# Kernel tuning notes

Measured on AMD Instinct MI355X. Metric: run time of the kernel, lower is better.

The kernel has to match this reference:

```python
import jax, jax.numpy as jnp
import numpy as np

N = 4096
FEAT = 5
H = 128
L = 3
K = 4
HD = H // K  # 32


def setup_inputs() -> dict:
    key = jax.random.key(0)
    ks = jax.random.split(key, 24)
    node_features = jax.random.normal(ks[0], (N, FEAT), dtype=jnp.float32)
    u = jax.random.uniform(ks[1], (N, N), dtype=jnp.float32)
    adj = jnp.where(u < 0.01, u, 0.0)
    adj = adj / (adj.sum(axis=1, keepdims=True) + 1e-8)  # row-normalised
    mask = jax.random.randint(ks[2], (N,), 0, 2).astype(bool)
    s = 0.05
    return {
        'node_features': node_features,
        'adj': adj,
        'mask': mask,
        'Wi': jax.random.normal(ks[3], (FEAT, H), jnp.float32) * s,
        'bi': jnp.zeros((H,), jnp.float32),
        'gat_W': jax.random.normal(ks[4], (L, K, H, HD), jnp.float32) * s,
        'gat_a': jax.random.normal(ks[5], (L, K, 2 * HD), jnp.float32) * s,
        'ln_g': jnp.ones((L, H), jnp.float32),
        'ln_b': jnp.zeros((L, H), jnp.float32),
        'pW1': jax.random.normal(ks[6], (H, H // 2), jnp.float32) * s,
        'pb1': jnp.zeros((H // 2,), jnp.float32),
        'pW2': jax.random.normal(ks[7], (H // 2, 1), jnp.float32) * s,
        'pb2': jnp.zeros((1,), jnp.float32),
        'poolW': jax.random.normal(ks[8], (H, H), jnp.float32) * s,
        'poolb': jnp.zeros((H,), jnp.float32),
        'poolv': jax.random.normal(ks[9], (H,), jnp.float32) * s,
        'vW1': jax.random.normal(ks[10], (H, H // 2), jnp.float32) * s,
        'vb1': jnp.zeros((H // 2,), jnp.float32),
        'vW2': jax.random.normal(ks[11], (H // 2, 1), jnp.float32) * s,
        'vb2': jnp.zeros((1,), jnp.float32),
    }


def _layernorm(x, g, b, eps=1e-5):
    mu = x.mean(-1, keepdims=True)
    var = ((x - mu) ** 2).mean(-1, keepdims=True)
    return (x - mu) / jnp.sqrt(var + eps) * g + b


def reference(node_features, adj, mask, Wi, bi, gat_W, gat_a, ln_g, ln_b,
              pW1, pb1, pW2, pb2, poolW, poolb, poolv, vW1, vb1, vW2, vb2):
    n = node_features.shape[0]
    x = jax.nn.relu(node_features @ Wi + bi)  # (N, H)
    edge_mask = (adj > 0) | jnp.eye(n, dtype=bool)  # (N, N) incl self-loops
    n_layers = gat_W.shape[0]
    for l in range(n_layers):
        Wx = jnp.einsum('nd,kdh->knh', x, gat_W[l])  # (K, N, hd)
        a_src = jnp.einsum('knh,kh->kn', Wx, gat_a[l][:, :HD])  # (K, N)
        a_dst = jnp.einsum('knh,kh->kn', Wx, gat_a[l][:, HD:])  # (K, N)
        e = jax.nn.leaky_relu(a_src[:, :, None] + a_dst[:, None, :], 0.2)  # (K,N,N)
        e = jnp.where(edge_mask[None], e, -jnp.inf)
        alpha = jax.nn.softmax(e, axis=-1)  # softmax over neighbours j
        h = jax.nn.elu(jnp.einsum('kij,kjh->kih', alpha, Wx))  # (K, N, hd)
        out = jnp.transpose(h, (1, 0, 2)).reshape(n, -1)  # concat heads -> (N, H)
        out = out + x  # residual (Identity: in_dim == out_dim)
        x = _layernorm(out, ln_g[l], ln_b[l])
    # policy head
    logits = (jax.nn.relu(x @ pW1 + pb1) @ pW2 + pb2).squeeze(-1)  # (N,)
    logits = jnp.where(mask, logits, -jnp.inf)
    # attention pooling restricted to masked (valid) nodes
    scores = jnp.tanh(x @ poolW + poolb) @ poolv  # (N,)
    scores = jnp.where(mask, scores, -jnp.inf)
    beta = jax.nn.softmax(scores)
    pooled = (beta[:, None] * x).sum(0)  # (H,)
    value = (jax.nn.relu(pooled @ vW1 + vb1) @ vW2 + vb2).squeeze(-1)  # scalar
    return logits, value
```

## Files before the change

### kernel.cpp

```cpp
#include <hip/hip_runtime.h>

#define NN 4096
#define FEAT 5
#define H 128
#define HD 32
#define KH 4
#define NEG_INF (-__builtin_inff())
#define MASK_SENTINEL (-1e30f)

#define WS_FLAG  0
#define WS_DEG   256
#define WS_NBR   (WS_DEG + NN*4)
#define WS_X     (WS_NBR + NN*128*2)
#define WS_WX    (WS_X + NN*H*4)
#define WS_ATS   (WS_WX + KH*NN*HD*4)
#define WS_ATD   (WS_ATS + NN*16)
#define WS_PART  (WS_ATD + NN*16)
#define WS_ZPART (WS_PART + 256*H*4)

__device__ __forceinline__ float red64(float v) {
#pragma unroll
    for (int off = 32; off; off >>= 1) v += __shfl_xor(v, off, 64);
    return v;
}
__device__ __forceinline__ float red32(float v) {
#pragma unroll
    for (int off = 16; off; off >>= 1) v += __shfl_xor(v, off, 32);
    return v;
}
__device__ __forceinline__ float red32max(float v) {
#pragma unroll
    for (int off = 16; off; off >>= 1) v = fmaxf(v, __shfl_xor(v, off, 32));
    return v;
}
__device__ __forceinline__ bool read_mask(const void* mp, int f, int n) {
    if (f == 3) return ((const long long*)mp)[n] != 0;
    if (f == 1) return ((const int*)mp)[n] != 0;
    if (f == 2) return ((const float*)mp)[n] != 0.f;
    return ((const unsigned char*)mp)[n] != 0;
}

__global__ __launch_bounds__(256) void k_proj(
    const float* __restrict__ nf, const float* __restrict__ Wi,
    const float* __restrict__ bi, const void* mask, int* flag,
    float* __restrict__ xbuf) {
    int w = threadIdx.x >> 6, lane = threadIdx.x & 63;
    int n = blockIdx.x * 4 + w;
    float a1 = bi[lane], a2 = bi[64 + lane];
#pragma unroll
    for (int f = 0; f < FEAT; f++) {
        float xv = nf[n * FEAT + f];
        a1 += xv * Wi[f * H + lane];
        a2 += xv * Wi[f * H + 64 + lane];
    }
    xbuf[(size_t)n * H + lane] = fmaxf(a1, 0.f);
    xbuf[(size_t)n * H + 64 + lane] = fmaxf(a2, 0.f);
    if (blockIdx.x == 0 && w == 0) {
        const unsigned* ip = (const unsigned*)mask;
        const float* fp = (const float*)mask;
        bool i32ok = true, i64ok = true, f32ok = true;
        for (int i = lane; i < 1024; i += 64) {
            unsigned v = ip[i];
            if (v > 1u) i32ok = false;
            if (i & 1) { if (v != 0u) i64ok = false; }
            else       { if (v > 1u) i64ok = false; }
            float fv = fp[i];
            if (fv != 0.f && fv != 1.f) f32ok = false;
        }
        i32ok = (__ballot((int)i32ok) == ~0ull);
        i64ok = (__ballot((int)i64ok) == ~0ull);
        f32ok = (__ballot((int)f32ok) == ~0ull);
        if (lane == 0) *flag = i64ok ? 3 : (i32ok ? 1 : (f32ok ? 2 : 0));
    }
}

__global__ __launch_bounds__(256) void k_csr(
    const float* __restrict__ adj, int* __restrict__ deg,
    unsigned short* __restrict__ nbr) {
    __shared__ int ln[4][128];
    int w = threadIdx.x >> 6, lane = threadIdx.x & 63;
    int row = blockIdx.x * 4 + w;
    ln[w][lane] = 0; ln[w][64 + lane] = 0;
    const float4* arow = (const float4*)(adj + (size_t)row * NN);
    int cnt = 0;
    bool self = false;
    for (int c0 = 0; c0 < NN / 4; c0 += 64) {
        float4 v = arow[c0 + lane];
        int cb = (c0 + lane) * 4;
        float vals[4] = {v.x, v.y, v.z, v.w};
#pragma unroll
        for (int s = 0; s < 4; s++) {
            bool nz = vals[s] > 0.f;
            if (nz && cb + s == row) self = true;
            unsigned long long b = __ballot((int)nz);
            if (nz) {
                int pos = cnt + __popcll(b & ((1ull << lane) - 1ull));
                if (pos < 128) ln[w][pos] = cb + s;
            }
            cnt += __popcll(b);
        }
    }
    bool anyself = __any((int)self);
    if (!anyself) {
        if (lane == 0 && cnt < 128) ln[w][cnt] = row;
        cnt++;
    }
    int d = cnt < 128 ? cnt : 128;
    if (lane == 0) deg[row] = d;
    nbr[(size_t)row * 128 + lane] = (unsigned short)ln[w][lane];
    nbr[(size_t)row * 128 + 64 + lane] = (unsigned short)ln[w][64 + lane];
}

__global__ __launch_bounds__(256) void k_wx(
    const float* __restrict__ xbuf, const float* __restrict__ gw,
    const float* __restrict__ ga, float* __restrict__ Wx,
    float* __restrict__ attS, float* __restrict__ attD) {
    __shared__ float xs[8][H];
    int t = threadIdx.x;
    int k = t >> 6, lane = t & 63, dh = lane >> 5, h = lane & 31;
    int n0 = blockIdx.x * 8;
    ((float4*)xs)[t] = ((const float4*)(xbuf + (size_t)n0 * H))[t];
    __syncthreads();
    float acc[8] = {0, 0, 0, 0, 0, 0, 0, 0};
    const float* g = gw + (size_t)k * (H * HD) + h;
    for (int dd = 0; dd < 64; dd += 4) {
        int d = dh * 64 + dd;
        float w0 = g[(size_t)(d + 0) * HD];
        float w1 = g[(size_t)(d + 1) * HD];
        float w2 = g[(size_t)(d + 2) * HD];
        float w3 = g[(size_t)(d + 3) * HD];
#pragma unroll
        for (int nn = 0; nn < 8; nn++) {
            float4 xv = *(const float4*)&xs[nn][d];
            acc[nn] += xv.x * w0 + xv.y * w1 + xv.z * w2 + xv.w * w3;
        }
    }
    float aws = ga[k * 64 + h], awd = ga[k * 64 + 32 + h];
#pragma unroll
    for (int nn = 0; nn < 8; nn++) {
        float full = acc[nn] + __shfl_xor(acc[nn], 32, 64);
        float s = red32(full * aws);
        float dv = red32(full * awd);
        int n = n0 + nn;
        if (dh == 0) Wx[(size_t)k * NN * HD + (size_t)n * HD + h] = full;
        if (lane == 0) { attS[n * 4 + k] = s; attD[n * 4 + k] = dv; }
    }
}

__global__ __launch_bounds__(256) void k_agg(
    const int* __restrict__ degG, const unsigned short* __restrict__ nbrG,
    const float* __restrict__ Wx, const float4* __restrict__ attS4,
    const float4* __restrict__ attD4, const float* __restrict__ lng,
    const float* __restrict__ lnb, float* __restrict__ xbuf) {
    __shared__ int lds_nbr[4][128];
    __shared__ float lds_al[4][2][128];
    __shared__ float lds_red[2][2][2];
    int t = threadIdx.x, w = t >> 6, lane = t & 63;
    int nn = w >> 1, wp = w & 1;
    int node = blockIdx.x * 2 + nn;
    int hs = lane >> 5, h = lane & 31;
    int k = 2 * wp + hs;
    int d = degG[node];
    {
        const unsigned short* np = nbrG + (size_t)node * 128;
        ushort2 a = *(const ushort2*)(np + lane * 2);
        lds_nbr[w][lane * 2] = a.x;
        lds_nbr[w][lane * 2 + 1] = a.y;
    }
    float4 aSv = attS4[node];
    float ai = wp ? (hs ? aSv.w : aSv.z) : (hs ? aSv.y : aSv.x);
    float e[4];
#pragma unroll
    for (int r = 0; r < 4; r++) {
        int c = r * 32 + h;
        if (c < d) {
            float4 dv4 = attD4[lds_nbr[w][c]];
            float dvv = wp ? (hs ? dv4.w : dv4.z) : (hs ? dv4.y : dv4.x);
            float v = ai + dvv;
            e[r] = v > 0.f ? v : 0.2f * v;
        } else e[r] = NEG_INF;
    }
    float m = red32max(fmaxf(fmaxf(e[0], e[1]), fmaxf(e[2], e[3])));
    float p[4], s = 0.f;
#pragma unroll
    for (int r = 0; r < 4; r++) {
        p[r] = (r * 32 + h < d) ? __expf(e[r] - m) : 0.f;
        s += p[r];
    }
    s = red32(s);
    float inv = 1.f / s;
#pragma unroll
    for (int r = 0; r < 4; r++) lds_al[w][hs][r * 32 + h] = p[r] * inv;
    float acc = 0.f;
    const float* wxk = Wx + (size_t)k * NN * HD + h;
    const float* ap = lds_al[w][hs];
    const int* np2 = lds_nbr[w];
    int dpad = (d + 7) & ~7;
    for (int c0 = 0; c0 < dpad; c0 += 8) {
        float a0 = ap[c0], a1 = ap[c0+1], a2 = ap[c0+2], a3 = ap[c0+3];
        float a4 = ap[c0+4], a5 = ap[c0+5], a6 = ap[c0+6], a7 = ap[c0+7];
        int s0 = np2[c0], s1 = np2[c0+1], s2 = np2[c0+2], s3 = np2[c0+3];
        int s4 = np2[c0+4], s5 = np2[c0+5], s6 = np2[c0+6], s7 = np2[c0+7];
        float v0 = wxk[(size_t)s0 * HD], v1 = wxk[(size_t)s1 * HD];
        float v2 = wxk[(size_t)s2 * HD], v3 = wxk[(size_t)s3 * HD];
        float v4 = wxk[(size_t)s4 * HD], v5 = wxk[(size_t)s5 * HD];
        float v6 = wxk[(size_t)s6 * HD], v7 = wxk[(size_t)s7 * HD];
        acc += a0*v0 + a1*v1 + a2*v2 + a3*v3 + a4*v4 + a5*v5 + a6*v6 + a7*v7;
    }
    float hv = acc > 0.f ? acc : __expf(acc) - 1.f;
    int dim = wp * 64 + lane;
    float o = hv + xbuf[(size_t)node * H + dim];
    float ps = red64(o);
    if (lane == 0) lds_red[nn][wp][0] = ps;
    __syncthreads();
    float mu = (lds_red[nn][0][0] + lds_red[nn][1][0]) * (1.f / H);
    float dv = o - mu;
    float vs = red64(dv * dv);
    if (lane == 0) lds_red[nn][wp][1] = vs;
    __syncthreads();
    float var = (lds_red[nn][0][1] + lds_red[nn][1][1]) * (1.f / H);
    float rstd = rsqrtf(var + 1e-5f);
    xbuf[(size_t)node * H + dim] = dv * rstd * lng[dim] + lnb[dim];
}

__global__ __launch_bounds__(256) void k_heads(
    const float* __restrict__ xbuf, const float* __restrict__ pW1,
    const float* __restrict__ pb1, const float* __restrict__ pW2,
    const float* __restrict__ pb2, const float* __restrict__ poolW,
    const float* __restrict__ poolb, const float* __restrict__ poolv,
    const void* mask, const int* __restrict__ flag, float* __restrict__ out,
    float* __restrict__ part, float* __restrict__ zpart) {
    __shared__ float lds_x[16][H];
    __shared__ float lds_part[4][H];
    __shared__ float lds_z[4];
    int t = threadIdx.x, w = t >> 6, lane = t & 63;
    int n0b = blockIdx.x * 16;
    for (int idx = t; idx < 16 * H; idx += 256)
        lds_x[idx >> 7][idx & 127] = xbuf[(size_t)(n0b + (idx >> 7)) * H + (idx & 127)];
    __syncthreads();
    int nb = n0b + w * 4;
    float accp[4] = {0, 0, 0, 0}, acs1[4] = {0, 0, 0, 0}, acs2[4] = {0, 0, 0, 0};
#pragma unroll 2
    for (int d = 0; d < H; d++) {
        float w1 = pW1[d * 64 + lane];
        float q1 = poolW[d * H + lane];
        float q2 = poolW[d * H + 64 + lane];
#pragma unroll
        for (int nn = 0; nn < 4; nn++) {
            float xv = lds_x[w * 4 + nn][d];
            accp[nn] += xv * w1;
            acs1[nn] += xv * q1;
            acs2[nn] += xv * q2;
        }
    }
    int flg = *flag;
    float T = fminf(red64(fabsf(poolv[lane]) + fabsf(poolv[64 + lane])), 30.f);
    float pb1v = pb1[lane], pw2v = pW2[lane], pb2v = pb2[0];
    float pob1 = poolb[lane], pob2 = poolb[64 + lane];
    float pov1 = poolv[lane], pov2 = poolv[64 + lane];
    float pp1 = 0.f, pp2 = 0.f, zacc = 0.f;
#pragma unroll
    for (int nn = 0; nn < 4; nn++) {
        int node = nb + nn;
        float hp = red64(fmaxf(accp[nn] + pb1v, 0.f) * pw2v);
        float sc = red64(tanhf(acs1[nn] + pob1) * pov1 + tanhf(acs2[nn] + pob2) * pov2);
        bool mk = read_mask(mask, flg, node);
        if (lane == 0) out[node] = mk ? (hp + pb2v) : MASK_SENTINEL;
        float wn = mk ? __expf(sc - T) : 0.f;
        pp1 += wn * lds_x[w * 4 + nn][lane];
        pp2 += wn * lds_x[w * 4 + nn][64 + lane];
        zacc += wn;
    }
    lds_part[w][lane] = pp1;
    lds_part[w][64 + lane] = pp2;
    if (lane == 0) lds_z[w] = zacc;
    __syncthreads();
    if (w == 0) {
        float s1 = lds_part[0][lane] + lds_part[1][lane] + lds_part[2][lane] + lds_part[3][lane];
        float s2 = lds_part[0][64 + lane] + lds_part[1][64 + lane] +
                   lds_part[2][64 + lane] + lds_part[3][64 + lane];
        part[blockIdx.x * H + lane] = s1;
        part[blockIdx.x * H + 64 + lane] = s2;
        if (lane == 0) zpart[blockIdx.x] = lds_z[0] + lds_z[1] + lds_z[2] + lds_z[3];
    }
}

__global__ __launch_bounds__(1024) void k_value(
    const float* __restrict__ part, const float* __restrict__ zpart,
    const float* __restrict__ vW1, const float* __restrict__ vb1,
    const float* __restrict__ vW2, const float* __restrict__ vb2,
    float* __restrict__ out) {
    __shared__ float segsum[8][H];
    __shared__ float zfin[256];
    __shared__ float pooled[H];
    int t = threadIdx.x;
    int dim = t & 127, seg = t >> 7;
    float s = 0.f;
#pragma unroll 8
    for (int b = seg * 32; b < seg * 32 + 32; b++) s += part[b * H + dim];
    segsum[seg][dim] = s;
    if (t < 256) zfin[t] = zpart[t];
    __syncthreads();
    if (t < 512) {
        int sg = t >> 7;
        segsum[sg][dim] += segsum[sg + 4][dim];
    }
    if (t >= 512 && t < 640) zfin[t - 512] += zfin[t - 512 + 128];
    __syncthreads();
    if (t < 256) {
        int sg = t >> 7;
        segsum[sg][dim] += segsum[sg + 2][dim];
    }
    if (t >= 512 && t < 576) zfin[t - 512] += zfin[t - 512 + 64];
    __syncthreads();
    if (t < 128) segsum[0][dim] += segsum[1][dim];
    if (t >= 512 && t < 544) zfin[t - 512] += zfin[t - 512 + 32];
    __syncthreads();
    if (t < 32) {
        float z = zfin[t];
#pragma unroll
        for (int off = 16; off; off >>= 1) z += __shfl_xor(z, off, 32);
        if (t == 0) zfin[0] = z;
    }
    __syncthreads();
    float Z = zfin[0];
    if (t < H) pooled[t] = segsum[0][t] / Z;
    __syncthreads();
    if (t < 64) {
        float acc = vb1[t];
#pragma unroll 4
        for (int d = 0; d < H; d++) acc += pooled[d] * vW1[d * 64 + t];
        float v = red64(fmaxf(acc, 0.f) * vW2[t]);
        if (t == 0) out[NN] = v + vb2[0];
    }
}

extern "C" void kernel_launch(void* const* d_in, const int* in_sizes, int n_in,
                              void* d_out, int out_size, void* d_ws, size_t ws_size,
                              hipStream_t stream) {
    const float* nf    = (const float*)d_in[0];
    const float* adj   = (const float*)d_in[1];
    const void*  mask  = d_in[2];
    const float* Wi    = (const float*)d_in[3];
    const float* bi    = (const float*)d_in[4];
    const float* gat_W = (const float*)d_in[5];
    const float* gat_a = (const float*)d_in[6];
    const float* ln_g  = (const float*)d_in[7];
    const float* ln_b  = (const float*)d_in[8];
    const float* pW1   = (const float*)d_in[9];
    const float* pb1   = (const float*)d_in[10];
    const float* pW2   = (const float*)d_in[11];
    const float* pb2   = (const float*)d_in[12];
    const float* poolW = (const float*)d_in[13];
    const float* poolb = (const float*)d_in[14];
    const float* poolv = (const float*)d_in[15];
    const float* vW1   = (const float*)d_in[16];
    const float* vb1   = (const float*)d_in[17];
    const float* vW2   = (const float*)d_in[18];
    const float* vb2   = (const float*)d_in[19];

    char* ws = (char*)d_ws;
    int*            flag = (int*)(ws + WS_FLAG);
    int*            deg  = (int*)(ws + WS_DEG);
    unsigned short* nbr  = (unsigned short*)(ws + WS_NBR);
    float* xbuf  = (float*)(ws + WS_X);
    float* Wx    = (float*)(ws + WS_WX);
    float* ats   = (float*)(ws + WS_ATS);
    float* atd   = (float*)(ws + WS_ATD);
    float* partb = (float*)(ws + WS_PART);
    float* zpart = (float*)(ws + WS_ZPART);
    float* out   = (float*)d_out;

    const size_t GWL = KH * H * HD;
    const size_t GAL = KH * 2 * HD;

    k_proj<<<1024, 256, 0, stream>>>(nf, Wi, bi, mask, flag, xbuf);
    k_csr<<<1024, 256, 0, stream>>>(adj, deg, nbr);
    for (int l = 0; l < 3; l++) {
        k_wx<<<512, 256, 0, stream>>>(xbuf, gat_W + l * GWL, gat_a + l * GAL,
                                      Wx, ats, atd);
        k_agg<<<2048, 256, 0, stream>>>(deg, nbr, Wx, (const float4*)ats,
                                        (const float4*)atd, ln_g + l * H,
                                        ln_b + l * H, xbuf);
    }
    k_heads<<<256, 256, 0, stream>>>(xbuf, pW1, pb1, pW2, pb2, poolW, poolb, poolv,
                                     mask, flag, out, partb, zpart);
    k_value<<<1, 1024, 0, stream>>>(partb, zpart, vW1, vb1, vW2, vb2, out);
}
```

Measured before the change: 145.6 us.

## Fuse CSR build with input projection and remap aggregation to one node per block

The input projection kernel is merged into the CSR-building kernel, which removes one launch. The GAT aggregation kernel now uses one block per node with one wave per head. Each wave computes a 128-wide softmax spread over 64 lanes and splits the neighbours between two half-waves, so attention weights come from shuffles instead of an LDS array and the pre-normalisation sum is scaled once at the end. This doubles the block count and adds block-level syncs and shuffles in the gather loop, in exchange for more parallelism per node and shorter serial neighbour loops.

```diff
diff --git a/kernel.cpp b/kernel.cpp
--- a/kernel.cpp
+++ b/kernel.cpp
@@ -23,14 +23,14 @@
     for (int off = 32; off; off >>= 1) v += __shfl_xor(v, off, 64);
     return v;
 }
+__device__ __forceinline__ float red64max(float v) {
+#pragma unroll
+    for (int off = 32; off; off >>= 1) v = fmaxf(v, __shfl_xor(v, off, 64));
+    return v;
+}
 __device__ __forceinline__ float red32(float v) {
 #pragma unroll
     for (int off = 16; off; off >>= 1) v += __shfl_xor(v, off, 32);
-    return v;
-}
-__device__ __forceinline__ float red32max(float v) {
-#pragma unroll
-    for (int off = 16; off; off >>= 1) v = fmaxf(v, __shfl_xor(v, off, 32));
     return v;
 }
 __device__ __forceinline__ bool read_mask(const void* mp, int f, int n) {
@@ -40,21 +40,52 @@
     return ((const unsigned char*)mp)[n] != 0;
 }
 
-__global__ __launch_bounds__(256) void k_proj(
-    const float* __restrict__ nf, const float* __restrict__ Wi,
-    const float* __restrict__ bi, const void* mask, int* flag,
-    float* __restrict__ xbuf) {
+__global__ __launch_bounds__(256) void k_csr_proj(
+    const float* __restrict__ adj, const float* __restrict__ nf,
+    const float* __restrict__ Wi, const float* __restrict__ bi,
+    const void* mask, int* flag, int* __restrict__ deg,
+    unsigned short* __restrict__ nbr, float* __restrict__ xbuf) {
+    __shared__ int ln[4][128];
     int w = threadIdx.x >> 6, lane = threadIdx.x & 63;
-    int n = blockIdx.x * 4 + w;
+    int row = blockIdx.x * 4 + w;
+    ln[w][lane] = 0; ln[w][64 + lane] = 0;
+    const float4* arow = (const float4*)(adj + (size_t)row * NN);
+    int cnt = 0;
+    bool self = false;
+    for (int c0 = 0; c0 < NN / 4; c0 += 64) {
+        float4 v = arow[c0 + lane];
+        int cb = (c0 + lane) * 4;
+        float vals[4] = {v.x, v.y, v.z, v.w};
+#pragma unroll
+        for (int s = 0; s < 4; s++) {
+            bool nz = vals[s] > 0.f;
+            if (nz && cb + s == row) self = true;
+            unsigned long long b = __ballot((int)nz);
+            if (nz) {
+                int pos = cnt + __popcll(b & ((1ull << lane) - 1ull));
+                if (pos < 128) ln[w][pos] = cb + s;
+            }
+            cnt += __popcll(b);
+        }
+    }
+    bool anyself = __any((int)self);
+    if (!anyself) {
+        if (lane == 0 && cnt < 128) ln[w][cnt] = row;
+        cnt++;
+    }
+    int d = cnt < 128 ? cnt : 128;
+    if (lane == 0) deg[row] = d;
+    nbr[(size_t)row * 128 + lane] = (unsigned short)ln[w][lane];
+    nbr[(size_t)row * 128 + 64 + lane] = (unsigned short)ln[w][64 + lane];
     float a1 = bi[lane], a2 = bi[64 + lane];
 #pragma unroll
     for (int f = 0; f < FEAT; f++) {
-        float xv = nf[n * FEAT + f];
+        float xv = nf[row * FEAT + f];
         a1 += xv * Wi[f * H + lane];
         a2 += xv * Wi[f * H + 64 + lane];
     }
-    xbuf[(size_t)n * H + lane] = fmaxf(a1, 0.f);
-    xbuf[(size_t)n * H + 64 + lane] = fmaxf(a2, 0.f);
+    xbuf[(size_t)row * H + lane] = fmaxf(a1, 0.f);
+    xbuf[(size_t)row * H + 64 + lane] = fmaxf(a2, 0.f);
     if (blockIdx.x == 0 && w == 0) {
         const unsigned* ip = (const unsigned*)mask;
         const float* fp = (const float*)mask;
@@ -74,43 +105,6 @@
     }
 }
 
-__global__ __launch_bounds__(256) void k_csr(
-    const float* __restrict__ adj, int* __restrict__ deg,
-    unsigned short* __restrict__ nbr) {
-    __shared__ int ln[4][128];
-    int w = threadIdx.x >> 6, lane = threadIdx.x & 63;
-    int row = blockIdx.x * 4 + w;
-    ln[w][lane] = 0; ln[w][64 + lane] = 0;
-    const float4* arow = (const float4*)(adj + (size_t)row * NN);
-    int cnt = 0;
-    bool self = false;
-    for (int c0 = 0; c0 < NN / 4; c0 += 64) {
-        float4 v = arow[c0 + lane];
-        int cb = (c0 + lane) * 4;
-        float vals[4] = {v.x, v.y, v.z, v.w};
-#pragma unroll
-        for (int s = 0; s < 4; s++) {
-            bool nz = vals[s] > 0.f;
-            if (nz && cb + s == row) self = true;
-            unsigned long long b = __ballot((int)nz);
-            if (nz) {
-                int pos = cnt + __popcll(b & ((1ull << lane) - 1ull));
-                if (pos < 128) ln[w][pos] = cb + s;
-            }
-            cnt += __popcll(b);
-        }
-    }
-    bool anyself = __any((int)self);
-    if (!anyself) {
-        if (lane == 0 && cnt < 128) ln[w][cnt] = row;
-        cnt++;
-    }
-    int d = cnt < 128 ? cnt : 128;
-    if (lane == 0) deg[row] = d;
-    nbr[(size_t)row * 128 + lane] = (unsigned short)ln[w][lane];
-    nbr[(size_t)row * 128 + 64 + lane] = (unsigned short)ln[w][64 + lane];
-}
-
 __global__ __launch_bounds__(256) void k_wx(
     const float* __restrict__ xbuf, const float* __restrict__ gw,
     const float* __restrict__ ga, float* __restrict__ Wx,
@@ -152,75 +146,67 @@
     const float* __restrict__ Wx, const float4* __restrict__ attS4,
     const float4* __restrict__ attD4, const float* __restrict__ lng,
     const float* __restrict__ lnb, float* __restrict__ xbuf) {
-    __shared__ int lds_nbr[4][128];
-    __shared__ float lds_al[4][2][128];
-    __shared__ float lds_red[2][2][2];
+    __shared__ int s_nbr[128];
+    __shared__ float s_o[H];
+    __shared__ float s_red[2], s_red2[2];
     int t = threadIdx.x, w = t >> 6, lane = t & 63;
-    int nn = w >> 1, wp = w & 1;
-    int node = blockIdx.x * 2 + nn;
-    int hs = lane >> 5, h = lane & 31;
-    int k = 2 * wp + hs;
+    int node = blockIdx.x;
+    int k = w;
+    int h = lane & 31, q = lane >> 5;
     int d = degG[node];
-    {
-        const unsigned short* np = nbrG + (size_t)node * 128;
-        ushort2 a = *(const ushort2*)(np + lane * 2);
-        lds_nbr[w][lane * 2] = a.x;
-        lds_nbr[w][lane * 2 + 1] = a.y;
-    }
+    if (t < 128) s_nbr[t] = nbrG[(size_t)node * 128 + t];
+    __syncthreads();
     float4 aSv = attS4[node];
-    float ai = wp ? (hs ? aSv.w : aSv.z) : (hs ? aSv.y : aSv.x);
-    float e[4];
-#pragma unroll
-    for (int r = 0; r < 4; r++) {
-        int c = r * 32 + h;
-        if (c < d) {
-            float4 dv4 = attD4[lds_nbr[w][c]];
-            float dvv = wp ? (hs ? dv4.w : dv4.z) : (hs ? dv4.y : dv4.x);
-            float v = ai + dvv;
-            e[r] = v > 0.f ? v : 0.2f * v;
-        } else e[r] = NEG_INF;
-    }
-    float m = red32max(fmaxf(fmaxf(e[0], e[1]), fmaxf(e[2], e[3])));
-    float p[4], s = 0.f;
-#pragma unroll
-    for (int r = 0; r < 4; r++) {
-        p[r] = (r * 32 + h < d) ? __expf(e[r] - m) : 0.f;
-        s += p[r];
-    }
-    s = red32(s);
-    float inv = 1.f / s;
-#pragma unroll
-    for (int r = 0; r < 4; r++) lds_al[w][hs][r * 32 + h] = p[r] * inv;
+    float ai = k == 0 ? aSv.x : k == 1 ? aSv.y : k == 2 ? aSv.z : aSv.w;
+    float e0 = NEG_INF, e1 = NEG_INF;
+    if (lane < d) {
+        float4 dv4 = attD4[s_nbr[lane]];
+        float dvv = k == 0 ? dv4.x : k == 1 ? dv4.y : k == 2 ? dv4.z : dv4.w;
+        float v = ai + dvv;
+        e0 = v > 0.f ? v : 0.2f * v;
+    }
+    if (64 + lane < d) {
+        float4 dv4 = attD4[s_nbr[64 + lane]];
+        float dvv = k == 0 ? dv4.x : k == 1 ? dv4.y : k == 2 ? dv4.z : dv4.w;
+        float v = ai + dvv;
+        e1 = v > 0.f ? v : 0.2f * v;
+    }
+    float m = red64max(fmaxf(e0, e1));
+    float p0 = (lane < d) ? __expf(e0 - m) : 0.f;
+    float p1 = (64 + lane < d) ? __expf(e1 - m) : 0.f;
+    float inv = 1.f / red64(p0 + p1);
     float acc = 0.f;
     const float* wxk = Wx + (size_t)k * NN * HD + h;
-    const float* ap = lds_al[w][hs];
-    const int* np2 = lds_nbr[w];
-    int dpad = (d + 7) & ~7;
-    for (int c0 = 0; c0 < dpad; c0 += 8) {
-        float a0 = ap[c0], a1 = ap[c0+1], a2 = ap[c0+2], a3 = ap[c0+3];
-        float a4 = ap[c0+4], a5 = ap[c0+5], a6 = ap[c0+6], a7 = ap[c0+7];
-        int s0 = np2[c0], s1 = np2[c0+1], s2 = np2[c0+2], s3 = np2[c0+3];
-        int s4 = np2[c0+4], s5 = np2[c0+5], s6 = np2[c0+6], s7 = np2[c0+7];
-        float v0 = wxk[(size_t)s0 * HD], v1 = wxk[(size_t)s1 * HD];
-        float v2 = wxk[(size_t)s2 * HD], v3 = wxk[(size_t)s3 * HD];
-        float v4 = wxk[(size_t)s4 * HD], v5 = wxk[(size_t)s5 * HD];
-        float v6 = wxk[(size_t)s6 * HD], v7 = wxk[(size_t)s7 * HD];
-        acc += a0*v0 + a1*v1 + a2*v2 + a3*v3 + a4*v4 + a5*v5 + a6*v6 + a7*v7;
-    }
-    float hv = acc > 0.f ? acc : __expf(acc) - 1.f;
-    int dim = wp * 64 + lane;
-    float o = hv + xbuf[(size_t)node * H + dim];
+    int jmax = (d + 1) >> 1;
+#pragma unroll 4
+    for (int j = 0; j < jmax; j++) {
+        int c = 2 * j + q;
+        int sc = s_nbr[c];
+        float al = (c < 64) ? __shfl(p0, c, 64) : __shfl(p1, c - 64, 64);
+        acc += al * wxk[(size_t)sc * HD];
+    }
+    acc += __shfl_xor(acc, 32, 64);
+    if (lane < 32) {
+        float tot = acc * inv;
+        float hv = tot > 0.f ? tot : __expf(tot) - 1.f;
+        int dim = k * 32 + h;
+        s_o[dim] = hv + xbuf[(size_t)node * H + dim];
+    }
+    __syncthreads();
+    float o = (t < 128) ? s_o[t] : 0.f;
     float ps = red64(o);
-    if (lane == 0) lds_red[nn][wp][0] = ps;
-    __syncthreads();
-    float mu = (lds_red[nn][0][0] + lds_red[nn][1][0]) * (1.f / H);
+    if (lane == 0 && w < 2) s_red[w] = ps;
+    __syncthreads();
+    float mu = (s_red[0] + s_red[1]) * (1.f / H);
     float dv = o - mu;
-    float vs = red64(dv * dv);
-    if (lane == 0) lds_red[nn][wp][1] = vs;
-    __syncthreads();
-    float var = (lds_red[nn][0][1] + lds_red[nn][1][1]) * (1.f / H);
-    float rstd = rsqrtf(var + 1e-5f);
-    xbuf[(size_t)node * H + dim] = dv * rstd * lng[dim] + lnb[dim];
+    float vs = red64((t < 128) ? dv * dv : 0.f);
+    if (lane == 0 && w < 2) s_red2[w] = vs;
+    __syncthreads();
+    if (t < 128) {
+        float var = (s_red2[0] + s_red2[1]) * (1.f / H);
+        float rstd = rsqrtf(var + 1e-5f);
+        xbuf[(size_t)node * H + t] = dv * rstd * lng[t] + lnb[t];
+    }
 }
 
 __global__ __launch_bounds__(256) void k_heads(
@@ -374,12 +360,11 @@
     const size_t GWL = KH * H * HD;
     const size_t GAL = KH * 2 * HD;
 
-    k_proj<<<1024, 256, 0, stream>>>(nf, Wi, bi, mask, flag, xbuf);
-    k_csr<<<1024, 256, 0, stream>>>(adj, deg, nbr);
+    k_csr_proj<<<1024, 256, 0, stream>>>(adj, nf, Wi, bi, mask, flag, deg, nbr, xbuf);
     for (int l = 0; l < 3; l++) {
         k_wx<<<512, 256, 0, stream>>>(xbuf, gat_W + l * GWL, gat_a + l * GAL,
                                       Wx, ats, atd);
-        k_agg<<<2048, 256, 0, stream>>>(deg, nbr, Wx, (const float4*)ats,
+        k_agg<<<4096, 256, 0, stream>>>(deg, nbr, Wx, (const float4*)ats,
                                         (const float4*)atd, ln_g + l * H,
                                         ln_b + l * H, xbuf);
     }
```

Measured after the change: 178.0 us. +22.3%, slower.
